# Performance work log

Hardware: AMD Instinct MI355X
Metric: run time of the kernel (lower is better)

## Reference

```python
import jax, jax.numpy as jnp
import numpy as np


def _pairwise_adj(x):
    # exp(-||xi - xj||^2), shape [B, N, N]
    inner = -2.0 * jnp.einsum('bnd,bmd->bnm', x, x)
    sq = jnp.sum(x * x, axis=-1, keepdims=True)
    return jnp.exp(-(sq + inner + jnp.swapaxes(sq, 1, 2)))


def _knn_adj(adj, k):
    # keep top-k weights per row, zero elsewhere
    vals, idx = jax.lax.top_k(adj, k)
    b = jnp.arange(adj.shape[0])[:, None, None]
    n = jnp.arange(adj.shape[1])[None, :, None]
    return jnp.zeros_like(adj).at[b, n, idx].set(vals)


def _laplacian(adj):
    # normalized Laplacian L = I - D^-1/2 A D^-1/2
    d = jnp.sum(adj, axis=-1)
    dinv = jnp.where(d > 0, 1.0 / jnp.sqrt(d), 0.0)
    norm_adj = dinv[:, :, None] * adj * dinv[:, None, :]
    return jnp.eye(adj.shape[1], dtype=adj.dtype) - norm_adj


def _cheb_conv(x, L, W, b):
    # Chebyshev polynomial graph conv: sum_k T_k(L) x W_k + b
    K = W.shape[0]
    x0 = x
    out = jnp.einsum('bnf,fo->bno', x0, W[0])
    if K > 1:
        x1 = jnp.matmul(L, x0)
        out = out + jnp.einsum('bnf,fo->bno', x1, W[1])
        for kk in range(2, K):
            x2 = 2.0 * jnp.matmul(L, x1) - x0
            out = out + jnp.einsum('bnf,fo->bno', x2, W[kk])
            x0, x1 = x1, x2
    return out + b


def setup_inputs() -> dict:
    key = jax.random.key(0)
    ks = jax.random.split(key, 4)
    B, N, Fin, Fout, K, C = 16, 2048, 6, 128, 6, 40
    x = jax.random.normal(ks[0], (B, N, Fin), dtype=jnp.float32)
    sccs = jax.random.randint(ks[1], (B, 64, 16), 0, N)  # unused in one_layer branch
    W1 = jax.random.normal(ks[2], (K, Fin, Fout), dtype=jnp.float32) * 0.05
    b1 = jnp.zeros((Fout,), dtype=jnp.float32)
    fc_w = jax.random.normal(ks[3], (Fout, C), dtype=jnp.float32) * 0.05
    fc_b = jnp.zeros((C,), dtype=jnp.float32)
    return {"x": x, "k": 40, "batch_size": B, "num_points": N,
            "sccs": sccs, "W1": W1, "b1": b1, "fc_w": fc_w, "fc_b": fc_b}


def reference(x, k, batch_size, num_points, sccs, W1, b1, fc_w, fc_b):
    # graph built under no_grad in the original -> stop_gradient here
    L = jax.lax.stop_gradient(_laplacian(_knn_adj(_pairwise_adj(x), k)))
    out = jax.nn.relu(_cheb_conv(x, L, W1, b1))           # [B, N, 128]
    # reg_prior: ||out^T L out||_F ** 2
    M = jnp.einsum('bnf,bnm,bmg->bfg', out, L, out)       # [B, 128, 128]
    reg = jnp.sum(M * M)
    pooled = jnp.max(out, axis=1)                         # [B, 128]
    logits = pooled @ fc_w + fc_b                         # [B, class_num]
    return logits, reg
```

## Files before the change

### kernel.cpp

```cpp
#include <hip/hip_runtime.h>
#include <math.h>

#define BB   16
#define NN   2048
#define FIN  6
#define FOUT 128
#define KCH  6
#define KNN  40
#define NCLS 40

__global__ __launch_bounds__(512) void knn_kernel(const float* __restrict__ x,
                                                  int* __restrict__ topi,
                                                  float* __restrict__ topv,
                                                  float* __restrict__ dinv)
{
    __shared__ __align__(16) float xs[FIN][NN];
    __shared__ unsigned int   hist[8][64];
    __shared__ unsigned int   ck[8][64];
    __shared__ unsigned short ci[8][64];
    __shared__ unsigned int   ccnt[8];

    int bb   = blockIdx.x >> 5;
    int i0   = (blockIdx.x & 31) * 64;
    int t    = threadIdx.x;
    int lane = t & 63;
    int wv   = t >> 6;

    const float* xb = x + (size_t)bb * NN * FIN;
    for (int idx = t; idx < NN * FIN; idx += 512) {
        int j = idx / FIN, f = idx - j * FIN;
        xs[f][j] = xb[idx];
    }
    __syncthreads();

    for (int rr = 0; rr < 8; ++rr) {
        int i   = i0 + wv * 8 + rr;
        int row = bb * NN + i;

        float xi0 = xs[0][i], xi1 = xs[1][i], xi2 = xs[2][i],
              xi3 = xs[3][i], xi4 = xs[4][i], xi5 = xs[5][i];

        float d[32];
#pragma unroll
        for (int uu = 0; uu < 8; ++uu) {
            int j4 = uu * 64 + lane;
            float4 p0 = ((const float4*)xs[0])[j4];
            float4 p1 = ((const float4*)xs[1])[j4];
            float4 p2 = ((const float4*)xs[2])[j4];
            float4 p3 = ((const float4*)xs[3])[j4];
            float4 p4 = ((const float4*)xs[4])[j4];
            float4 p5 = ((const float4*)xs[5])[j4];
#define DNE(E, C)                                                                \
            { float q0 = p0.C - xi0, q1 = p1.C - xi1, q2 = p2.C - xi2,           \
                    q3 = p3.C - xi3, q4 = p4.C - xi4, q5 = p5.C - xi5;           \
              d[uu * 4 + E] = fmaf(q5,q5, fmaf(q4,q4, fmaf(q3,q3,                \
                              fmaf(q2,q2, fmaf(q1,q1, q0*q0)))));  }
            DNE(0, x) DNE(1, y) DNE(2, z) DNE(3, w)
#undef DNE
        }

        float lo = 0.0f, invw = 16.0f;
        int base = 0, pivot = 127;

        for (int pass = 0; pass < 6; ++pass) {
            hist[wv][lane] = 0u;
#pragma unroll
            for (int u = 0; u < 32; ++u) {
                float dv = d[u];
                if (dv >= lo) {
                    int bin = (int)((dv - lo) * invw);
                    if (bin < 128)
                        atomicAdd(&hist[wv][bin >> 1], 1u << ((bin & 1) << 4));
                }
            }
            unsigned int h = hist[wv][lane];
            int b0 = (int)(h & 0xFFFFu), b1 = (int)(h >> 16);
            int s = b0 + b1;
            int incl = s;
#pragma unroll
            for (int off = 1; off < 64; off <<= 1) {
                int up = __shfl_up(incl, off, 64);
                if (lane >= off) incl += up;
            }
            int total = __shfl(incl, 63, 64);

            if (base + total < KNN) {
                base += total;
                lo   += 128.0f / invw;
                invw *= 0.5f;
                continue;
            }

            unsigned long long ball = __ballot(base + incl >= KNN);
            int pl = __ffsll(ball) - 1;
            int p_ = 0, cb_ = 0, cs_ = 0;
            if (lane == pl) {
                int cbefore = base + incl - s;
                if (cbefore + b0 >= KNN) { p_ = pl * 2;     cb_ = cbefore;      cs_ = cbefore + b0; }
                else                     { p_ = pl * 2 + 1; cb_ = cbefore + b0; cs_ = cbefore + b0 + b1; }
            }
            pivot    = __shfl(p_, pl, 64);
            int cumb = __shfl(cb_, pl, 64);
            int csel = __shfl(cs_, pl, 64);

            if (csel <= 64) break;

            lo   = lo + (float)pivot / invw;
            invw *= 128.0f;
            base = cumb;
        }

        if (lane == 0) ccnt[wv] = 0u;
#pragma unroll
        for (int u = 0; u < 32; ++u) {
            int ib = (int)((d[u] - lo) * invw);
            if (ib <= pivot) {
                unsigned int slot = atomicAdd(&ccnt[wv], 1u);
                if (slot < 64u) {
                    ck[wv][slot] = __float_as_uint(d[u]);
                    ci[wv][slot] = (unsigned short)((u >> 2) * 256 + (lane << 2) + (u & 3));
                }
            }
        }
        unsigned int c = ccnt[wv];
        if (c > 64u) c = 64u;

        unsigned int kk = (lane < (int)c) ? ck[wv][lane] : 0xFFFFFFFFu;
        int          id = (lane < (int)c) ? (int)ci[wv][lane] : -1;

        int rank = 0;
        int cI = (int)c;
        for (int m = 0; m < cI; ++m) {
            unsigned int km = __shfl(kk, m, 64);
            rank += (km < kk || (km == kk && m < lane)) ? 1 : 0;
        }

        float ev = 0.0f;
        if (rank < KNN) {
            ev = expf(-__uint_as_float(kk));
            topv[(size_t)row * KNN + rank] = ev;
            topi[(size_t)row * KNN + rank] = id;
        }
        float ssum = ev;
#pragma unroll
        for (int off = 32; off; off >>= 1) ssum += __shfl_xor(ssum, off, 64);
        if (lane == 0) dinv[row] = 1.0f / sqrtf(ssum);
    }
}

__global__ __launch_bounds__(192) void cheb_apply(const float* __restrict__ xin,
                                                  const float* __restrict__ xsub,
                                                  float* __restrict__ xout,
                                                  const int* __restrict__ topi,
                                                  const float* __restrict__ wnrm,
                                                  const float* __restrict__ topv,
                                                  const float* __restrict__ dinv,
                                                  float* __restrict__ wnrm_out,
                                                  float scale)
{
    __shared__ int   si[32 * KNN];
    __shared__ float sw[32 * KNN];
    int r0 = blockIdx.x * 32;
    int t  = threadIdx.x;
    if (topv) {
        int b = r0 >> 11;
        const float* dv = dinv + ((size_t)b << 11);
        for (int l = t; l < 32 * KNN; l += 192) {
            size_t idx = (size_t)r0 * KNN + l;
            int j = topi[idx];
            float w = topv[idx] * dinv[r0 + l / KNN] * dv[j];
            si[l] = j; sw[l] = w;
            wnrm_out[idx] = w;
        }
    } else {
        for (int l = t; l < 32 * KNN; l += 192) {
            si[l] = topi[(size_t)r0 * KNN + l];
            sw[l] = wnrm[(size_t)r0 * KNN + l];
        }
    }
    __syncthreads();

    int rl = t / FIN, f = t - rl * FIN;
    int r  = r0 + rl;
    int b  = r >> 11;
    const float* xbase = xin + (size_t)b * NN * FIN + f;
    const int*   sip = si + rl * KNN;
    const float* swp = sw + rl * KNN;
    float a = xin[(size_t)r * FIN + f];
#pragma unroll 8
    for (int s = 0; s < KNN; ++s)
        a = fmaf(-swp[s], xbase[(size_t)sip[s] * FIN], a);
    a *= scale;
    if (xsub) a -= xsub[(size_t)r * FIN + f];
    xout[(size_t)r * FIN + f] = a;
}

__global__ __launch_bounds__(512) void chebout_kernel(const float* __restrict__ x,
                                                      const float* __restrict__ xks,
                                                      const float* __restrict__ W1,
                                                      const float* __restrict__ b1,
                                                      float* __restrict__ outb)
{
    __shared__ float W1s[KCH * FIN * FOUT];
    __shared__ float b1s[FOUT];
    __shared__ float xk[16][KCH * FIN];
    int r0 = blockIdx.x * 16;
    int t  = threadIdx.x;
    for (int l = t; l < KCH * FIN * FOUT; l += 512) W1s[l] = W1[l];
    if (t < FOUT) b1s[t] = b1[t];
    for (int l = t; l < 16 * KCH * FIN; l += 512) {
        int rl = l / (KCH * FIN), kf = l % (KCH * FIN);
        int k = kf / FIN, f = kf % FIN;
        int r = r0 + rl;
        xk[rl][kf] = (k == 0) ? x[(size_t)r * FIN + f]
                              : xks[(size_t)(k - 1) * BB * NN * FIN + (size_t)r * FIN + f];
    }
    __syncthreads();
    int fo = t & 127;
#pragma unroll
    for (int it = 0; it < 4; ++it) {
        int rl = (t >> 7) + it * 4;
        float acc = b1s[fo];
#pragma unroll
        for (int kf = 0; kf < KCH * FIN; ++kf)
            acc = fmaf(xk[rl][kf], W1s[kf * FOUT + fo], acc);
        outb[(size_t)(r0 + rl) * FOUT + fo] = fmaxf(acc, 0.0f);
    }
}

__global__ __launch_bounds__(1024) void loutmsq_kernel(const float* __restrict__ outb,
                                                       const int* __restrict__ topi,
                                                       const float* __restrict__ wnrm,
                                                       float* __restrict__ mchunk)
{
    int id  = blockIdx.x;
    int xcd = id & 7, k = id >> 3;
    int bb  = xcd + 8 * (k >> 4);
    int nch = k & 15;
    int t   = threadIdx.x;

    __shared__ __align__(16) float aT[64][FOUT];
    __shared__ __align__(16) float bT[64][FOUT];

    const float* ob = outb + (size_t)bb * NN * FOUT;
    float acc[4][4] = {{0.f}};
    int tx = t & 31, ty = t >> 5;
    int grl = t >> 4;
    int gfq = (t & 15) * 2;

    for (int st = 0; st < 2; ++st) {
        int n0 = nch * 128 + st * 64;
        {
            const float4* src = (const float4*)(ob + (size_t)n0 * FOUT);
            float4* dst = (float4*)aT;
            dst[t]        = src[t];
            dst[t + 1024] = src[t + 1024];
        }
        __syncthreads();
        {
            int r = n0 + grl;
            const int*   ti = topi + ((size_t)bb * NN + r) * KNN;
            const float* tw = wnrm + ((size_t)bb * NN + r) * KNN;
            float4 a0 = ((const float4*)aT[grl])[gfq];
            float4 a1 = ((const float4*)aT[grl])[gfq + 1];
#pragma unroll 8
            for (int s = 0; s < KNN; ++s) {
                int j = ti[s]; float w = tw[s];
                const float4* jr = (const float4*)(ob + (size_t)j * FOUT);
                float4 v0 = jr[gfq], v1 = jr[gfq + 1];
                a0.x = fmaf(-w, v0.x, a0.x); a0.y = fmaf(-w, v0.y, a0.y);
                a0.z = fmaf(-w, v0.z, a0.z); a0.w = fmaf(-w, v0.w, a0.w);
                a1.x = fmaf(-w, v1.x, a1.x); a1.y = fmaf(-w, v1.y, a1.y);
                a1.z = fmaf(-w, v1.z, a1.z); a1.w = fmaf(-w, v1.w, a1.w);
            }
            ((float4*)bT[grl])[gfq]     = a0;
            ((float4*)bT[grl])[gfq + 1] = a1;
        }
        __syncthreads();
#pragma unroll 8
        for (int qq = 0; qq < 64; ++qq) {
            float4 av = ((const float4*)aT[qq])[tx];
            float4 bv = ((const float4*)bT[qq])[ty];
            float af[4] = {av.x, av.y, av.z, av.w};
            float bg[4] = {bv.x, bv.y, bv.z, bv.w};
#pragma unroll
            for (int ii = 0; ii < 4; ++ii)
#pragma unroll
                for (int jj = 0; jj < 4; ++jj)
                    acc[ii][jj] = fmaf(af[ii], bg[jj], acc[ii][jj]);
        }
        __syncthreads();
    }
    size_t basem = ((size_t)bb * 16 + nch) << 14;
#pragma unroll
    for (int ii = 0; ii < 4; ++ii) {
        float4 v = make_float4(acc[ii][0], acc[ii][1], acc[ii][2], acc[ii][3]);
        *(float4*)&mchunk[basem + (size_t)(tx * 4 + ii) * FOUT + ty * 4] = v;
    }
}

__global__ __launch_bounds__(256) void mred_kernel(const float* __restrict__ mchunk,
                                                   float* __restrict__ mpart)
{
    int t = threadIdx.x;
    size_t E = ((size_t)blockIdx.x * 256 + t) * 4;
    int bb = (int)(E >> 14);
    int fg = (int)(E & 16383);
    float4 a = make_float4(0.f, 0.f, 0.f, 0.f);
    for (int c = 0; c < 16; ++c) {
        float4 v = *(const float4*)&mchunk[((size_t)(bb * 16 + c) << 14) + fg];
        a.x += v.x; a.y += v.y; a.z += v.z; a.w += v.w;
    }
    float s = a.x * a.x + a.y * a.y + a.z * a.z + a.w * a.w;
#pragma unroll
    for (int off = 32; off; off >>= 1) s += __shfl_down(s, off, 64);
    __shared__ float ws[4];
    if ((t & 63) == 0) ws[t >> 6] = s;
    __syncthreads();
    if (t == 0) mpart[blockIdx.x] = ws[0] + ws[1] + ws[2] + ws[3];
}

__global__ __launch_bounds__(128) void pmax_kernel(const float* __restrict__ outb,
                                                   float* __restrict__ pmax)
{
    int c = blockIdx.x, b = blockIdx.y, t = threadIdx.x;
    const float* ob = outb + ((size_t)b * NN + (size_t)c * 128) * FOUT;
    float m = -3.0e38f;
#pragma unroll 4
    for (int n = 0; n < 128; ++n) m = fmaxf(m, ob[(size_t)n * FOUT + t]);
    pmax[((size_t)b * 16 + c) * FOUT + t] = m;
}

__global__ __launch_bounds__(128) void logits_kernel(const float* __restrict__ pmax,
                                                     const float* __restrict__ fcw,
                                                     const float* __restrict__ fcb,
                                                     float* __restrict__ dout)
{
    int b = blockIdx.x, t = threadIdx.x;
    __shared__ float pooled[FOUT];
    float m = pmax[((size_t)b * 16 + 0) * FOUT + t];
    for (int c = 1; c < 16; ++c) m = fmaxf(m, pmax[((size_t)b * 16 + c) * FOUT + t]);
    pooled[t] = m;
    __syncthreads();
    if (t < NCLS) {
        float acc = fcb[t];
        for (int f = 0; f < FOUT; ++f) acc = fmaf(pooled[f], fcw[f * NCLS + t], acc);
        dout[b * NCLS + t] = acc;
    }
}

__global__ __launch_bounds__(256) void reg_kernel(const float* __restrict__ mpart,
                                                  float* __restrict__ dout)
{
    int t = threadIdx.x;
    float s = mpart[t];
#pragma unroll
    for (int off = 32; off; off >>= 1) s += __shfl_down(s, off, 64);
    __shared__ float ws[4];
    if ((t & 63) == 0) ws[t >> 6] = s;
    __syncthreads();
    if (t == 0) dout[0] = ws[0] + ws[1] + ws[2] + ws[3];
}

extern "C" void kernel_launch(void* const* d_in, const int* in_sizes, int n_in,
                              void* d_out, int out_size, void* d_ws, size_t ws_size,
                              hipStream_t stream)
{
    const float* x   = (const float*)d_in[0];
    const float* W1  = (const float*)d_in[5];
    const float* b1  = (const float*)d_in[6];
    const float* fcw = (const float*)d_in[7];
    const float* fcb = (const float*)d_in[8];

    char* p = (char*)d_ws;
    auto alloc = [&](size_t bytes) { void* q = (void*)p; p += (bytes + 255) & ~(size_t)255; return q; };
    int*   topi   = (int*)  alloc((size_t)BB * NN * KNN * 4);
    float* topv   = (float*)alloc((size_t)BB * NN * KNN * 4);
    float* dinv   = (float*)alloc((size_t)BB * NN * 4);
    float* wnrm   = (float*)alloc((size_t)BB * NN * KNN * 4);
    float* xks    = (float*)alloc((size_t)5 * BB * NN * FIN * 4);
    float* outb   = (float*)alloc((size_t)BB * NN * FOUT * 4);
    float* mchunk = (float*)alloc((size_t)BB * 16 * FOUT * FOUT * 4);
    float* mpart  = (float*)alloc(256 * 4);
    float* pmax   = (float*)alloc((size_t)BB * 16 * FOUT * 4);

    const size_t ST = (size_t)BB * NN * FIN;

    knn_kernel<<<512, 512, 0, stream>>>(x, topi, topv, dinv);

    cheb_apply<<<1024, 192, 0, stream>>>(x,            nullptr,      xks + 0 * ST, topi, nullptr, topv, dinv, wnrm, 1.0f);
    cheb_apply<<<1024, 192, 0, stream>>>(xks + 0 * ST, x,            xks + 1 * ST, topi, wnrm, nullptr, nullptr, nullptr, 2.0f);
    cheb_apply<<<1024, 192, 0, stream>>>(xks + 1 * ST, xks + 0 * ST, xks + 2 * ST, topi, wnrm, nullptr, nullptr, nullptr, 2.0f);
    cheb_apply<<<1024, 192, 0, stream>>>(xks + 2 * ST, xks + 1 * ST, xks + 3 * ST, topi, wnrm, nullptr, nullptr, nullptr, 2.0f);
    cheb_apply<<<1024, 192, 0, stream>>>(xks + 3 * ST, xks + 2 * ST, xks + 4 * ST, topi, wnrm, nullptr, nullptr, nullptr, 2.0f);

    chebout_kernel<<<BB * NN / 16, 512, 0, stream>>>(x, xks, W1, b1, outb);
    loutmsq_kernel<<<256, 1024, 0, stream>>>(outb, topi, wnrm, mchunk);
    mred_kernel<<<256, 256, 0, stream>>>(mchunk, mpart);
    pmax_kernel<<<dim3(16, 16), 128, 0, stream>>>(outb, pmax);
    logits_kernel<<<BB, 128, 0, stream>>>(pmax, fcw, fcb, (float*)d_out);
    reg_kernel<<<1, 256, 0, stream>>>(mpart, (float*)d_out + BB * NCLS);
}
```

Measured before the change: 240.6 us.

## Use norm-expansion distances in kNN and fuse max-pooling into chebout via atomicMax

```diff
diff --git a/kernel.cpp b/kernel.cpp
--- a/kernel.cpp
+++ b/kernel.cpp
@@ -15,8 +15,9 @@
                                                   float* __restrict__ dinv)
 {
     __shared__ __align__(16) float xs[FIN][NN];
+    __shared__ __align__(16) float cs[NN];
     __shared__ unsigned int   hist[8][64];
-    __shared__ unsigned int   ck[8][64];
+    __shared__ float          ck[8][64];
     __shared__ unsigned short ci[8][64];
     __shared__ unsigned int   ccnt[8];
 
@@ -32,6 +33,13 @@
         xs[f][j] = xb[idx];
     }
     __syncthreads();
+    for (int j = t; j < NN; j += 512) {
+        float s0 = xs[0][j], s1 = xs[1][j], s2 = xs[2][j],
+              s3 = xs[3][j], s4 = xs[4][j], s5 = xs[5][j];
+        cs[j] = fmaf(s5,s5, fmaf(s4,s4, fmaf(s3,s3,
+                fmaf(s2,s2, fmaf(s1,s1, s0*s0)))));
+    }
+    __syncthreads();
 
     for (int rr = 0; rr < 8; ++rr) {
         int i   = i0 + wv * 8 + rr;
@@ -39,6 +47,7 @@
 
         float xi0 = xs[0][i], xi1 = xs[1][i], xi2 = xs[2][i],
               xi3 = xs[3][i], xi4 = xs[4][i], xi5 = xs[5][i];
+        float si  = cs[i];
 
         float d[32];
 #pragma unroll
@@ -50,16 +59,16 @@
             float4 p3 = ((const float4*)xs[3])[j4];
             float4 p4 = ((const float4*)xs[4])[j4];
             float4 p5 = ((const float4*)xs[5])[j4];
+            float4 c4 = ((const float4*)cs)[j4];
 #define DNE(E, C)                                                                \
-            { float q0 = p0.C - xi0, q1 = p1.C - xi1, q2 = p2.C - xi2,           \
-                    q3 = p3.C - xi3, q4 = p4.C - xi4, q5 = p5.C - xi5;           \
-              d[uu * 4 + E] = fmaf(q5,q5, fmaf(q4,q4, fmaf(q3,q3,                \
-                              fmaf(q2,q2, fmaf(q1,q1, q0*q0)))));  }
+            { float dt = fmaf(p5.C, xi5, fmaf(p4.C, xi4, fmaf(p3.C, xi3,         \
+                         fmaf(p2.C, xi2, fmaf(p1.C, xi1, p0.C * xi0)))));        \
+              d[uu * 4 + E] = fmaf(-2.0f, dt, c4.C); }
             DNE(0, x) DNE(1, y) DNE(2, z) DNE(3, w)
 #undef DNE
         }
 
-        float lo = 0.0f, invw = 16.0f;
+        float lo = -si, invw = 16.0f;
         int base = 0, pivot = 127;
 
         for (int pass = 0; pass < 6; ++pass) {
@@ -117,7 +126,7 @@
             if (ib <= pivot) {
                 unsigned int slot = atomicAdd(&ccnt[wv], 1u);
                 if (slot < 64u) {
-                    ck[wv][slot] = __float_as_uint(d[u]);
+                    ck[wv][slot] = d[u];
                     ci[wv][slot] = (unsigned short)((u >> 2) * 256 + (lane << 2) + (u & 3));
                 }
             }
@@ -125,19 +134,19 @@
         unsigned int c = ccnt[wv];
         if (c > 64u) c = 64u;
 
-        unsigned int kk = (lane < (int)c) ? ck[wv][lane] : 0xFFFFFFFFu;
-        int          id = (lane < (int)c) ? (int)ci[wv][lane] : -1;
+        float kk = (lane < (int)c) ? ck[wv][lane] : 3.0e38f;
+        int   id = (lane < (int)c) ? (int)ci[wv][lane] : -1;
 
         int rank = 0;
         int cI = (int)c;
         for (int m = 0; m < cI; ++m) {
-            unsigned int km = __shfl(kk, m, 64);
+            float km = __shfl(kk, m, 64);
             rank += (km < kk || (km == kk && m < lane)) ? 1 : 0;
         }
 
         float ev = 0.0f;
         if (rank < KNN) {
-            ev = expf(-__uint_as_float(kk));
+            ev = expf(-(kk + si));
             topv[(size_t)row * KNN + rank] = ev;
             topi[(size_t)row * KNN + rank] = id;
         }
@@ -199,11 +208,13 @@
                                                       const float* __restrict__ xks,
                                                       const float* __restrict__ W1,
                                                       const float* __restrict__ b1,
-                                                      float* __restrict__ outb)
+                                                      float* __restrict__ outb,
+                                                      float* __restrict__ pmax)
 {
     __shared__ float W1s[KCH * FIN * FOUT];
     __shared__ float b1s[FOUT];
     __shared__ float xk[16][KCH * FIN];
+    __shared__ float mx[4][FOUT];
     int r0 = blockIdx.x * 16;
     int t  = threadIdx.x;
     for (int l = t; l < KCH * FIN * FOUT; l += 512) W1s[l] = W1[l];
@@ -217,6 +228,7 @@
     }
     __syncthreads();
     int fo = t & 127;
+    float om = 0.0f;
 #pragma unroll
     for (int it = 0; it < 4; ++it) {
         int rl = (t >> 7) + it * 4;
@@ -224,7 +236,16 @@
 #pragma unroll
         for (int kf = 0; kf < KCH * FIN; ++kf)
             acc = fmaf(xk[rl][kf], W1s[kf * FOUT + fo], acc);
-        outb[(size_t)(r0 + rl) * FOUT + fo] = fmaxf(acc, 0.0f);
+        float o = fmaxf(acc, 0.0f);
+        outb[(size_t)(r0 + rl) * FOUT + fo] = o;
+        om = fmaxf(om, o);
+    }
+    mx[t >> 7][fo] = om;
+    __syncthreads();
+    if (t < FOUT) {
+        float m = fmaxf(fmaxf(mx[0][t], mx[1][t]), fmaxf(mx[2][t], mx[3][t]));
+        int b = r0 >> 11;
+        atomicMax((unsigned int*)&pmax[(size_t)b * FOUT + t], __float_as_uint(m));
     }
 }
 
@@ -320,17 +341,6 @@
     if (t == 0) mpart[blockIdx.x] = ws[0] + ws[1] + ws[2] + ws[3];
 }
 
-__global__ __launch_bounds__(128) void pmax_kernel(const float* __restrict__ outb,
-                                                   float* __restrict__ pmax)
-{
-    int c = blockIdx.x, b = blockIdx.y, t = threadIdx.x;
-    const float* ob = outb + ((size_t)b * NN + (size_t)c * 128) * FOUT;
-    float m = -3.0e38f;
-#pragma unroll 4
-    for (int n = 0; n < 128; ++n) m = fmaxf(m, ob[(size_t)n * FOUT + t]);
-    pmax[((size_t)b * 16 + c) * FOUT + t] = m;
-}
-
 __global__ __launch_bounds__(128) void logits_kernel(const float* __restrict__ pmax,
                                                      const float* __restrict__ fcw,
                                                      const float* __restrict__ fcb,
@@ -338,9 +348,7 @@
 {
     int b = blockIdx.x, t = threadIdx.x;
     __shared__ float pooled[FOUT];
-    float m = pmax[((size_t)b * 16 + 0) * FOUT + t];
-    for (int c = 1; c < 16; ++c) m = fmaxf(m, pmax[((size_t)b * 16 + c) * FOUT + t]);
-    pooled[t] = m;
+    pooled[t] = pmax[(size_t)b * FOUT + t];
     __syncthreads();
     if (t < NCLS) {
         float acc = fcb[t];
@@ -382,9 +390,11 @@
     float* outb   = (float*)alloc((size_t)BB * NN * FOUT * 4);
     float* mchunk = (float*)alloc((size_t)BB * 16 * FOUT * FOUT * 4);
     float* mpart  = (float*)alloc(256 * 4);
-    float* pmax   = (float*)alloc((size_t)BB * 16 * FOUT * 4);
+    float* pmax   = (float*)alloc((size_t)BB * FOUT * 4);
 
     const size_t ST = (size_t)BB * NN * FIN;
+
+    hipMemsetAsync(pmax, 0, (size_t)BB * FOUT * 4, stream);
 
     knn_kernel<<<512, 512, 0, stream>>>(x, topi, topv, dinv);
 
@@ -394,10 +404,9 @@
     cheb_apply<<<1024, 192, 0, stream>>>(xks + 2 * ST, xks + 1 * ST, xks + 3 * ST, topi, wnrm, nullptr, nullptr, nullptr, 2.0f);
     cheb_apply<<<1024, 192, 0, stream>>>(xks + 3 * ST, xks + 2 * ST, xks + 4 * ST, topi, wnrm, nullptr, nullptr, nullptr, 2.0f);
 
-    chebout_kernel<<<BB * NN / 16, 512, 0, stream>>>(x, xks, W1, b1, outb);
+    chebout_kernel<<<BB * NN / 16, 512, 0, stream>>>(x, xks, W1, b1, outb, pmax);
     loutmsq_kernel<<<256, 1024, 0, stream>>>(outb, topi, wnrm, mchunk);
     mred_kernel<<<256, 256, 0, stream>>>(mchunk, mpart);
-    pmax_kernel<<<dim3(16, 16), 128, 0, stream>>>(outb, pmax);
     logits_kernel<<<BB, 128, 0, stream>>>(pmax, fcw, fcb, (float*)d_out);
     reg_kernel<<<1, 256, 0, stream>>>(mpart, (float*)d_out + BB * NCLS);
 }
```

Result: slower. 287.8 us (+19.6%).
